# Kernel tuning notes

Measured on AMD Instinct MI355X. Metric: run time of the kernel, lower is better.

The kernel has to match this reference:

```python
import jax, jax.numpy as jnp
import numpy as np

D_MODEL = 768
N_HEADS = 12
HEAD = 64
B, T = 2, 2048


def setup_inputs() -> dict:
    key = jax.random.key(0)
    k1, k2, k3 = jax.random.split(key, 3)
    x = jax.random.normal(k1, (B, T, D_MODEL), dtype=jnp.float32)
    W1 = jax.random.normal(k2, (3 * D_MODEL, D_MODEL), dtype=jnp.float32) * (1.0 / np.sqrt(D_MODEL))
    b1 = jnp.zeros((3 * D_MODEL,), dtype=jnp.float32)
    W2 = jax.random.normal(k3, (D_MODEL, D_MODEL), dtype=jnp.float32) * (1.0 / np.sqrt(D_MODEL))
    b2 = jnp.zeros((D_MODEL,), dtype=jnp.float32)
    return {"x": x, "W1": W1, "b1": b1, "W2": W2, "b2": b2}


def reference(x, W1, b1, W2, b2):
    Bx, Tx, C = x.shape
    qkv = jnp.einsum('btc,fc->btf', x, W1) + b1            # (B,T,3C)
    q, k, v = jnp.split(qkv, 3, axis=-1)
    # (B,T,H,Dh) -> (B,H,T,Dh)
    q = q.reshape(Bx, Tx, N_HEADS, HEAD).transpose(0, 2, 1, 3)
    k = k.reshape(Bx, Tx, N_HEADS, HEAD).transpose(0, 2, 1, 3)
    v = v.reshape(Bx, Tx, N_HEADS, HEAD).transpose(0, 2, 1, 3)
    scale = 1.0 / np.sqrt(HEAD)
    scores = jnp.einsum('bhqd,bhkd->bhqk', q, k) * scale   # (B,H,T,T)
    causal = jnp.tril(jnp.ones((Tx, Tx), dtype=bool))
    scores = jnp.where(causal, scores, jnp.finfo(scores.dtype).min)
    attn = jax.nn.softmax(scores, axis=-1)
    o = jnp.einsum('bhqk,bhkd->bhqd', attn, v)             # (B,H,T,Dh)
    o = o.transpose(0, 2, 1, 3).reshape(Bx, Tx, C)
    return jnp.einsum('btc,fc->btf', o, W2) + b2
```

## Files before the change

### kernel.cpp

```cpp
#include <hip/hip_runtime.h>


typedef float f32x4 __attribute__((ext_vector_type(4)));
typedef __bf16 bf16x8 __attribute__((ext_vector_type(8)));

#define D_MODEL 768
#define F3 2304
#define NHEADS 12
#define HEAD 64
#define BB 2
#define TT 2048
#define MROWS (BB*TT)
#define KDIM 768
#define LOG2E 1.44269504f
#define NX (MROWS*D_MODEL)
#define NW1 (F3*KDIM)
#define NW2 (D_MODEL*KDIM)

__device__ __forceinline__ unsigned short f2bf(float f) {
    unsigned int u = __float_as_uint(f);
    u += 0x7fffu + ((u >> 16) & 1u);
    return (unsigned short)(u >> 16);
}
__device__ __forceinline__ unsigned int pack2bf(float a, float b) {
    unsigned int ua = __float_as_uint(a), ub = __float_as_uint(b);
    ua += 0x7fffu + ((ua >> 16) & 1u);
    ub += 0x7fffu + ((ub >> 16) & 1u);
    return (ua >> 16) | (ub & 0xffff0000u);
}

__device__ __forceinline__ void async_copy16(unsigned short* lds, const unsigned short* g) {
    __builtin_amdgcn_global_load_lds(
        (const __attribute__((address_space(1))) unsigned int*)(const void*)g,
        (__attribute__((address_space(3))) unsigned int*)(void*)lds,
        16, 0, 0);
}

__global__ void prep(const float* __restrict__ x, const float* __restrict__ W1,
                     const float* __restrict__ W2, unsigned short* __restrict__ xb,
                     unsigned short* __restrict__ w1b, unsigned short* __restrict__ w2b) {
    const int i4 = (blockIdx.x * blockDim.x + threadIdx.x) * 4;
    const float* src; unsigned short* dst; int off;
    if (i4 < NX)                { src = x;  dst = xb;  off = i4; }
    else if (i4 < NX + NW1)     { src = W1; dst = w1b; off = i4 - NX; }
    else if (i4 < NX + NW1 + NW2) { src = W2; dst = w2b; off = i4 - NX - NW1; }
    else return;
    float4 v = *(const float4*)(src + off);
    uint2 o;
    o.x = pack2bf(v.x, v.y);
    o.y = pack2bf(v.z, v.w);
    *(uint2*)(dst + off) = o;
}

template<int EPI>
__global__ __launch_bounds__(256, 4) void gemm_bt(
    const unsigned short* __restrict__ A, const unsigned short* __restrict__ Bw,
    const float* __restrict__ bias, int K,
    float* __restrict__ Cout,
    unsigned short* __restrict__ Qb, unsigned short* __restrict__ Kb,
    unsigned short* __restrict__ VT)
{
    __shared__ unsigned short As[128*64];
    __shared__ unsigned short Bs[128*64];
    const int tid  = threadIdx.x;
    const int wave = tid >> 6;
    const int lane = tid & 63;
    const int quad = lane >> 4;
    const int l16  = lane & 15;
    const int m0 = blockIdx.x * 128;
    const int n0 = blockIdx.y * 128;
    const int wm = (wave >> 1) * 64;
    const int wn = (wave & 1) * 64;

    f32x4 acc[4][4] = {};

    const unsigned short* Ablk = A + (size_t)m0 * K;
    const unsigned short* Bblk = Bw + (size_t)n0 * K;
    const int srow = (lane >> 3);
    const int scol = ((lane & 7) ^ srow) * 8;

    for (int k0 = 0; k0 < K; k0 += 64) {
        #pragma unroll
        for (int q2 = 0; q2 < 4; ++q2) {
            int t = wave * 4 + q2;
            int row = t * 8 + srow;
            async_copy16(As + t * 512, Ablk + (size_t)row * K + k0 + scol);
            async_copy16(Bs + t * 512, Bblk + (size_t)row * K + k0 + scol);
        }
        asm volatile("s_waitcnt vmcnt(0)" ::: "memory");
        __syncthreads();

        #pragma unroll
        for (int kc2 = 0; kc2 < 2; ++kc2) {
            const int pos = ((kc2*4 + quad) ^ (l16 & 7)) * 8;
            bf16x8 a[4], b[4];
            #pragma unroll
            for (int i = 0; i < 4; ++i)
                a[i] = *(const bf16x8*)(As + (wm + i*16 + l16)*64 + pos);
            #pragma unroll
            for (int j = 0; j < 4; ++j)
                b[j] = *(const bf16x8*)(Bs + (wn + j*16 + l16)*64 + pos);
            #pragma unroll
            for (int i = 0; i < 4; ++i)
                #pragma unroll
                for (int j = 0; j < 4; ++j)
                    acc[i][j] = __builtin_amdgcn_mfma_f32_16x16x32_bf16(a[i], b[j], acc[i][j], 0, 0, 0);
        }
        __syncthreads();
    }

    if (EPI == 1) {
        #pragma unroll
        for (int j = 0; j < 4; ++j) {
            const int n = n0 + wn + j*16 + l16;
            const float bv = bias[n];
            #pragma unroll
            for (int i = 0; i < 4; ++i)
                #pragma unroll
                for (int r = 0; r < 4; ++r) {
                    const int m = m0 + wm + i*16 + quad*4 + r;
                    Cout[(size_t)m * D_MODEL + n] = acc[i][j][r] + bv;
                }
        }
    } else {
        const int seg = blockIdx.y / 6;
        if (seg < 2) {
            #pragma unroll
            for (int j = 0; j < 4; ++j) {
                const int n = n0 + wn + j*16 + l16;
                const float bv = bias[n];
                const int f = n - seg * 768;
                const int h = f >> 6, d = f & 63;
                #pragma unroll
                for (int i = 0; i < 4; ++i)
                    #pragma unroll
                    for (int r = 0; r < 4; ++r) {
                        const int m = m0 + wm + i*16 + quad*4 + r;
                        const int b = m >> 11, t = m & 2047;
                        const size_t idx = (((size_t)(b*NHEADS + h)) * TT + t) * HEAD + d;
                        const float v = acc[i][j][r] + bv;
                        if (seg == 0) Qb[idx] = f2bf(v * (0.125f * LOG2E));
                        else          Kb[idx] = f2bf(v);
                    }
            }
        } else {
            #pragma unroll
            for (int j = 0; j < 4; ++j) {
                const int n = n0 + wn + j*16 + l16;
                const float bv = bias[n];
                const int f = n - 1536;
                const int h = f >> 6, d = f & 63;
                #pragma unroll
                for (int i = 0; i < 4; ++i) {
                    const int m = m0 + wm + i*16 + quad*4;
                    const int b = m >> 11, t = m & 2047;
                    uint2 pk;
                    pk.x = pack2bf(acc[i][j][0] + bv, acc[i][j][1] + bv);
                    pk.y = pack2bf(acc[i][j][2] + bv, acc[i][j][3] + bv);
                    *(uint2*)(VT + ((size_t)(b*NHEADS + h) * HEAD + d) * TT + t) = pk;
                }
            }
        }
    }
}

__global__ __launch_bounds__(256, 3) void attn(
    const unsigned short* __restrict__ Qb, const unsigned short* __restrict__ Kb,
    const unsigned short* __restrict__ VT, unsigned short* __restrict__ Ob)
{
    __shared__ unsigned short Ks[128*64];
    __shared__ unsigned short Vt[64*128];
    __shared__ unsigned short Ps[4][16*128];

    const int tid  = threadIdx.x;
    const int wave = tid >> 6;
    const int lane = tid & 63;
    const int quad = lane >> 4;
    const int l16  = lane & 15;
    const int qt = (blockIdx.x + blockIdx.y) & 15;
    const int bh = blockIdx.y;
    const size_t hbase = (size_t)bh * TT * HEAD;

    bf16x8 qreg[2][2];
    #pragma unroll
    for (int g = 0; g < 2; ++g) {
        const unsigned short* qp = Qb + hbase
            + (size_t)(qt*128 + g*64 + wave*16 + l16) * HEAD + quad*8;
        qreg[g][0] = *(const bf16x8*)(qp);
        qreg[g][1] = *(const bf16x8*)(qp + 32);
    }

    const int krow8 = tid >> 3;
    const int kchunk = ((tid & 7) ^ (krow8 & 7)) * 8;
    const int vrow16 = tid >> 4;
    const int vchunk = ((tid & 15) ^ (vrow16 & 7)) * 8;

    f32x4 oacc[2][4] = {};
    float lst[2] = {0.f, 0.f};
    const int nkt = qt + 1;

    for (int kt = 0; kt < nkt; ++kt) {
        __syncthreads();

        const unsigned short* ksrc = Kb + hbase + (size_t)kt * 128 * HEAD;
        #pragma unroll
        for (int i = 0; i < 4; ++i)
            async_copy16(Ks + i*2048 + tid*8,
                         ksrc + (size_t)(i*32 + krow8) * 64 + kchunk);
        const unsigned short* vsrc = VT + hbase + kt * 128;
        #pragma unroll
        for (int i = 0; i < 4; ++i)
            async_copy16(Vt + i*2048 + tid*8,
                         vsrc + (size_t)(i*16 + vrow16) * TT + vchunk);
        asm volatile("s_waitcnt vmcnt(0)" ::: "memory");
        __syncthreads();

        #pragma unroll
        for (int g = 0; g < 2; ++g) {
            f32x4 s[8] = {};
            #pragma unroll
            for (int kc2 = 0; kc2 < 2; ++kc2) {
                bf16x8 bq = qreg[g][kc2];
                const int pos = ((kc2*4 + quad) ^ (l16 & 7)) * 8;
                #pragma unroll
                for (int nt = 0; nt < 8; ++nt) {
                    bf16x8 ak = *(const bf16x8*)(Ks + (nt*16 + l16)*64 + pos);
                    s[nt] = __builtin_amdgcn_mfma_f32_16x16x32_bf16(ak, bq, s[nt], 0, 0, 0);
                }
            }

            if (kt == qt) {
                const int ql = g*64 + wave*16 + l16;
                #pragma unroll
                for (int nt = 0; nt < 8; ++nt)
                    #pragma unroll
                    for (int r = 0; r < 4; ++r)
                        if (nt*16 + quad*4 + r > ql) s[nt][r] = -1e30f;
            }

            float rsum = 0.f;
            uint2 pck[8];
            #pragma unroll
            for (int nt = 0; nt < 8; ++nt) {
                const float p0 = exp2f(s[nt][0]);
                const float p1 = exp2f(s[nt][1]);
                const float p2 = exp2f(s[nt][2]);
                const float p3 = exp2f(s[nt][3]);
                rsum += (p0 + p1) + (p2 + p3);
                pck[nt].x = (__float_as_uint(p0) >> 16) | (__float_as_uint(p1) & 0xffff0000u);
                pck[nt].y = (__float_as_uint(p2) >> 16) | (__float_as_uint(p3) & 0xffff0000u);
            }
            rsum += __shfl_xor(rsum, 16);
            rsum += __shfl_xor(rsum, 32);
            lst[g] += rsum;

            #pragma unroll
            for (int nt = 0; nt < 8; ++nt)
                *(uint2*)(&Ps[wave][l16*128
                    + ((nt*2 + (quad>>1)) ^ (l16 & 7))*8 + (quad&1)*4]) = pck[nt];

            #pragma unroll
            for (int kc = 0; kc < 4; ++kc) {
                const int pos = ((kc*4 + quad) ^ (l16 & 7)) * 8;
                bf16x8 ap = *(const bf16x8*)(&Ps[wave][l16*128 + pos]);
                #pragma unroll
                for (int dt = 0; dt < 4; ++dt) {
                    bf16x8 bv = *(const bf16x8*)(Vt + (dt*16 + l16)*128 + pos);
                    oacc[g][dt] = __builtin_amdgcn_mfma_f32_16x16x32_bf16(ap, bv, oacc[g][dt], 0, 0, 0);
                }
            }
        }
    }

    const int b = bh / NHEADS, h = bh % NHEADS;
    #pragma unroll
    for (int g = 0; g < 2; ++g) {
        const float linv = 1.0f / lst[g];
        float lr[4];
        #pragma unroll
        for (int r = 0; r < 4; ++r) lr[r] = __shfl(linv, quad*4 + r);
        #pragma unroll
        for (int r = 0; r < 4; ++r) {
            const int m = b * TT + qt*128 + g*64 + wave*16 + quad*4 + r;
            #pragma unroll
            for (int dt = 0; dt < 4; ++dt)
                Ob[(size_t)m * D_MODEL + h*HEAD + dt*16 + l16] = f2bf(oacc[g][dt][r] * lr[r]);
        }
    }
}

extern "C" void kernel_launch(void* const* d_in, const int* in_sizes, int n_in,
                              void* d_out, int out_size, void* d_ws, size_t ws_size,
                              hipStream_t stream) {
    const float* x  = (const float*)d_in[0];
    const float* W1 = (const float*)d_in[1];
    const float* b1 = (const float*)d_in[2];
    const float* W2 = (const float*)d_in[3];
    const float* b2 = (const float*)d_in[4];
    float* out = (float*)d_out;

    unsigned short* ws = (unsigned short*)d_ws;
    unsigned short* xb  = ws;
    unsigned short* w1b = xb  + (size_t)NX;
    unsigned short* w2b = w1b + (size_t)NW1;
    unsigned short* Qb  = w2b + (size_t)NW2;
    unsigned short* Kb  = Qb + (size_t)BB*NHEADS*TT*HEAD;
    unsigned short* VT  = Kb + (size_t)BB*NHEADS*TT*HEAD;
    unsigned short* Ob  = VT + (size_t)BB*NHEADS*TT*HEAD;

    prep<<<((NX + NW1 + NW2)/4 + 255)/256, 256, 0, stream>>>(x, W1, W2, xb, w1b, w2b);

    gemm_bt<0><<<dim3(MROWS/128, F3/128), 256, 0, stream>>>(
        xb, w1b, b1, KDIM, nullptr, Qb, Kb, VT);

    attn<<<dim3(TT/128, BB*NHEADS), 256, 0, stream>>>(Qb, Kb, VT, Ob);

    gemm_bt<1><<<dim3(MROWS/128, D_MODEL/128), 256, 0, stream>>>(
        Ob, w2b, b2, KDIM, out, nullptr, nullptr, nullptr);
}
```

Measured before the change: 177.9 us.

## Make attention waves independent, reading K/V directly from global memory

```diff
diff --git a/kernel.cpp b/kernel.cpp
--- a/kernel.cpp
+++ b/kernel.cpp
@@ -164,128 +164,103 @@
     }
 }
 
-__global__ __launch_bounds__(256, 3) void attn(
+__global__ __launch_bounds__(256, 4) void attn(
     const unsigned short* __restrict__ Qb, const unsigned short* __restrict__ Kb,
     const unsigned short* __restrict__ VT, unsigned short* __restrict__ Ob)
 {
-    __shared__ unsigned short Ks[128*64];
-    __shared__ unsigned short Vt[64*128];
-    __shared__ unsigned short Ps[4][16*128];
+    __shared__ unsigned short Ps[4][16*64];
 
     const int tid  = threadIdx.x;
     const int wave = tid >> 6;
     const int lane = tid & 63;
     const int quad = lane >> 4;
     const int l16  = lane & 15;
-    const int qt = (blockIdx.x + blockIdx.y) & 15;
     const int bh = blockIdx.y;
+    const int s  = wave*32 + ((blockIdx.x + blockIdx.y) & 31);
     const size_t hbase = (size_t)bh * TT * HEAD;
 
-    bf16x8 qreg[2][2];
+    unsigned short* ps = &Ps[wave][0];
+    const int psw = 2 * (l16 & 7);
+
+    bf16x8 q0, q1;
+    {
+        const unsigned short* qp = Qb + hbase + (size_t)(s*16 + l16) * HEAD + quad*8;
+        q0 = *(const bf16x8*)(qp);
+        q1 = *(const bf16x8*)(qp + 32);
+    }
+
+    f32x4 oacc[4] = {};
+    float lst = 0.f;
+    const int nkt = (s >> 2) + 1;
+
+    const unsigned short* kp0 = Kb + hbase + (size_t)l16 * HEAD + quad*8;
+    const unsigned short* vp0 = VT + hbase + (size_t)l16 * TT + quad*8;
+
+    for (int kt = 0; kt < nkt; ++kt) {
+        f32x4 sA[4] = {};
+        const unsigned short* kp = kp0 + (size_t)kt * 64 * HEAD;
+        #pragma unroll
+        for (int kc = 0; kc < 2; ++kc) {
+            const bf16x8 bq = kc ? q1 : q0;
+            #pragma unroll
+            for (int nt = 0; nt < 4; ++nt) {
+                bf16x8 ak = *(const bf16x8*)(kp + (size_t)nt*16*HEAD + kc*32);
+                sA[nt] = __builtin_amdgcn_mfma_f32_16x16x32_bf16(ak, bq, sA[nt], 0, 0, 0);
+            }
+        }
+
+        if (kt == nkt - 1) {
+            const int thr = s*16 + l16 - kt*64 - quad*4;
+            #pragma unroll
+            for (int nt = 0; nt < 4; ++nt)
+                #pragma unroll
+                for (int r = 0; r < 4; ++r)
+                    if (nt*16 + r > thr) sA[nt][r] = -1e30f;
+        }
+
+        float rsum = 0.f;
+        uint2 pck[4];
+        #pragma unroll
+        for (int nt = 0; nt < 4; ++nt) {
+            const float p0 = exp2f(sA[nt][0]);
+            const float p1 = exp2f(sA[nt][1]);
+            const float p2 = exp2f(sA[nt][2]);
+            const float p3 = exp2f(sA[nt][3]);
+            rsum += (p0 + p1) + (p2 + p3);
+            pck[nt].x = (__float_as_uint(p0) >> 16) | (__float_as_uint(p1) & 0xffff0000u);
+            pck[nt].y = (__float_as_uint(p2) >> 16) | (__float_as_uint(p3) & 0xffff0000u);
+        }
+        rsum += __shfl_xor(rsum, 16);
+        rsum += __shfl_xor(rsum, 32);
+        lst += rsum;
+
+        #pragma unroll
+        for (int nt = 0; nt < 4; ++nt)
+            *(uint2*)(ps + l16*64 + (((nt*4 + quad) ^ psw) * 4)) = pck[nt];
+
+        const unsigned short* vp = vp0 + kt*64;
+        #pragma unroll
+        for (int kc = 0; kc < 2; ++kc) {
+            bf16x8 ap = *(const bf16x8*)(ps + l16*64 + (((kc*8 + quad*2) ^ psw) * 4));
+            #pragma unroll
+            for (int dt = 0; dt < 4; ++dt) {
+                bf16x8 bv = *(const bf16x8*)(vp + (size_t)dt*16*TT + kc*32);
+                oacc[dt] = __builtin_amdgcn_mfma_f32_16x16x32_bf16(ap, bv, oacc[dt], 0, 0, 0);
+            }
+        }
+    }
+
+    const float linv = 1.0f / lst;
+    float lr[4];
     #pragma unroll
-    for (int g = 0; g < 2; ++g) {
-        const unsigned short* qp = Qb + hbase
-            + (size_t)(qt*128 + g*64 + wave*16 + l16) * HEAD + quad*8;
-        qreg[g][0] = *(const bf16x8*)(qp);
-        qreg[g][1] = *(const bf16x8*)(qp + 32);
-    }
-
-    const int krow8 = tid >> 3;
-    const int kchunk = ((tid & 7) ^ (krow8 & 7)) * 8;
-    const int vrow16 = tid >> 4;
-    const int vchunk = ((tid & 15) ^ (vrow16 & 7)) * 8;
-
-    f32x4 oacc[2][4] = {};
-    float lst[2] = {0.f, 0.f};
-    const int nkt = qt + 1;
-
-    for (int kt = 0; kt < nkt; ++kt) {
-        __syncthreads();
-
-        const unsigned short* ksrc = Kb + hbase + (size_t)kt * 128 * HEAD;
-        #pragma unroll
-        for (int i = 0; i < 4; ++i)
-            async_copy16(Ks + i*2048 + tid*8,
-                         ksrc + (size_t)(i*32 + krow8) * 64 + kchunk);
-        const unsigned short* vsrc = VT + hbase + kt * 128;
-        #pragma unroll
-        for (int i = 0; i < 4; ++i)
-            async_copy16(Vt + i*2048 + tid*8,
-                         vsrc + (size_t)(i*16 + vrow16) * TT + vchunk);
-        asm volatile("s_waitcnt vmcnt(0)" ::: "memory");
-        __syncthreads();
-
-        #pragma unroll
-        for (int g = 0; g < 2; ++g) {
-            f32x4 s[8] = {};
-            #pragma unroll
-            for (int kc2 = 0; kc2 < 2; ++kc2) {
-                bf16x8 bq = qreg[g][kc2];
-                const int pos = ((kc2*4 + quad) ^ (l16 & 7)) * 8;
-                #pragma unroll
-                for (int nt = 0; nt < 8; ++nt) {
-                    bf16x8 ak = *(const bf16x8*)(Ks + (nt*16 + l16)*64 + pos);
-                    s[nt] = __builtin_amdgcn_mfma_f32_16x16x32_bf16(ak, bq, s[nt], 0, 0, 0);
-                }
-            }
-
-            if (kt == qt) {
-                const int ql = g*64 + wave*16 + l16;
-                #pragma unroll
-                for (int nt = 0; nt < 8; ++nt)
-                    #pragma unroll
-                    for (int r = 0; r < 4; ++r)
-                        if (nt*16 + quad*4 + r > ql) s[nt][r] = -1e30f;
-            }
-
-            float rsum = 0.f;
-            uint2 pck[8];
-            #pragma unroll
-            for (int nt = 0; nt < 8; ++nt) {
-                const float p0 = exp2f(s[nt][0]);
-                const float p1 = exp2f(s[nt][1]);
-                const float p2 = exp2f(s[nt][2]);
-                const float p3 = exp2f(s[nt][3]);
-                rsum += (p0 + p1) + (p2 + p3);
-                pck[nt].x = (__float_as_uint(p0) >> 16) | (__float_as_uint(p1) & 0xffff0000u);
-                pck[nt].y = (__float_as_uint(p2) >> 16) | (__float_as_uint(p3) & 0xffff0000u);
-            }
-            rsum += __shfl_xor(rsum, 16);
-            rsum += __shfl_xor(rsum, 32);
-            lst[g] += rsum;
-
-            #pragma unroll
-            for (int nt = 0; nt < 8; ++nt)
-                *(uint2*)(&Ps[wave][l16*128
-                    + ((nt*2 + (quad>>1)) ^ (l16 & 7))*8 + (quad&1)*4]) = pck[nt];
-
-            #pragma unroll
-            for (int kc = 0; kc < 4; ++kc) {
-                const int pos = ((kc*4 + quad) ^ (l16 & 7)) * 8;
-                bf16x8 ap = *(const bf16x8*)(&Ps[wave][l16*128 + pos]);
-                #pragma unroll
-                for (int dt = 0; dt < 4; ++dt) {
-                    bf16x8 bv = *(const bf16x8*)(Vt + (dt*16 + l16)*128 + pos);
-                    oacc[g][dt] = __builtin_amdgcn_mfma_f32_16x16x32_bf16(ap, bv, oacc[g][dt], 0, 0, 0);
-                }
-            }
-        }
-    }
-
+    for (int r = 0; r < 4; ++r) lr[r] = __shfl(linv, quad*4 + r);
     const int b = bh / NHEADS, h = bh % NHEADS;
     #pragma unroll
-    for (int g = 0; g < 2; ++g) {
-        const float linv = 1.0f / lst[g];
-        float lr[4];
-        #pragma unroll
-        for (int r = 0; r < 4; ++r) lr[r] = __shfl(linv, quad*4 + r);
-        #pragma unroll
-        for (int r = 0; r < 4; ++r) {
-            const int m = b * TT + qt*128 + g*64 + wave*16 + quad*4 + r;
-            #pragma unroll
-            for (int dt = 0; dt < 4; ++dt)
-                Ob[(size_t)m * D_MODEL + h*HEAD + dt*16 + l16] = f2bf(oacc[g][dt][r] * lr[r]);
-        }
+    for (int r = 0; r < 4; ++r) {
+        const int m = b * TT + s*16 + quad*4 + r;
+        #pragma unroll
+        for (int dt = 0; dt < 4; ++dt)
+            Ob[(size_t)m * D_MODEL + h*HEAD + dt*16 + l16] = f2bf(oacc[dt][r] * lr[r]);
     }
 }
 
@@ -313,7 +288,7 @@
     gemm_bt<0><<<dim3(MROWS/128, F3/128), 256, 0, stream>>>(
         xb, w1b, b1, KDIM, nullptr, Qb, Kb, VT);
 
-    attn<<<dim3(TT/128, BB*NHEADS), 256, 0, stream>>>(Qb, Kb, VT, Ob);
+    attn<<<dim3(32, BB*NHEADS), 256, 0, stream>>>(Qb, Kb, VT, Ob);
 
     gemm_bt<1><<<dim3(MROWS/128, D_MODEL/128), 256, 0, stream>>>(
         Ob, w2b, b2, KDIM, out, nullptr, nullptr, nullptr);
```

New measurement: 211.9 us. 19.1% more time.

## Halve attention and output GEMM tile heights to raise block count

Applied to the files above, without the earlier changes.

```diff
diff --git a/kernel.cpp b/kernel.cpp
--- a/kernel.cpp
+++ b/kernel.cpp
@@ -52,11 +52,9 @@
     *(uint2*)(dst + off) = o;
 }
 
-template<int EPI>
-__global__ __launch_bounds__(256, 4) void gemm_bt(
+__global__ __launch_bounds__(256, 4) void gemm1(
     const unsigned short* __restrict__ A, const unsigned short* __restrict__ Bw,
     const float* __restrict__ bias, int K,
-    float* __restrict__ Cout,
     unsigned short* __restrict__ Qb, unsigned short* __restrict__ Kb,
     unsigned short* __restrict__ VT)
 {
@@ -109,62 +107,115 @@
         __syncthreads();
     }
 
-    if (EPI == 1) {
+    const int seg = blockIdx.y / 6;
+    if (seg < 2) {
         #pragma unroll
         for (int j = 0; j < 4; ++j) {
             const int n = n0 + wn + j*16 + l16;
             const float bv = bias[n];
+            const int f = n - seg * 768;
+            const int h = f >> 6, d = f & 63;
             #pragma unroll
             for (int i = 0; i < 4; ++i)
                 #pragma unroll
                 for (int r = 0; r < 4; ++r) {
                     const int m = m0 + wm + i*16 + quad*4 + r;
-                    Cout[(size_t)m * D_MODEL + n] = acc[i][j][r] + bv;
+                    const int b = m >> 11, t = m & 2047;
+                    const size_t idx = (((size_t)(b*NHEADS + h)) * TT + t) * HEAD + d;
+                    const float v = acc[i][j][r] + bv;
+                    if (seg == 0) Qb[idx] = f2bf(v * (0.125f * LOG2E));
+                    else          Kb[idx] = f2bf(v);
                 }
         }
     } else {
-        const int seg = blockIdx.y / 6;
-        if (seg < 2) {
-            #pragma unroll
-            for (int j = 0; j < 4; ++j) {
-                const int n = n0 + wn + j*16 + l16;
-                const float bv = bias[n];
-                const int f = n - seg * 768;
-                const int h = f >> 6, d = f & 63;
+        #pragma unroll
+        for (int j = 0; j < 4; ++j) {
+            const int n = n0 + wn + j*16 + l16;
+            const float bv = bias[n];
+            const int f = n - 1536;
+            const int h = f >> 6, d = f & 63;
+            #pragma unroll
+            for (int i = 0; i < 4; ++i) {
+                const int m = m0 + wm + i*16 + quad*4;
+                const int b = m >> 11, t = m & 2047;
+                uint2 pk;
+                pk.x = pack2bf(acc[i][j][0] + bv, acc[i][j][1] + bv);
+                pk.y = pack2bf(acc[i][j][2] + bv, acc[i][j][3] + bv);
+                *(uint2*)(VT + ((size_t)(b*NHEADS + h) * HEAD + d) * TT + t) = pk;
+            }
+        }
+    }
+}
+
+__global__ __launch_bounds__(256, 4) void gemm2(
+    const unsigned short* __restrict__ A, const unsigned short* __restrict__ Bw,
+    const float* __restrict__ bias, int K, float* __restrict__ Cout)
+{
+    __shared__ unsigned short As[64*64];
+    __shared__ unsigned short Bs[128*64];
+    const int tid  = threadIdx.x;
+    const int wave = tid >> 6;
+    const int lane = tid & 63;
+    const int quad = lane >> 4;
+    const int l16  = lane & 15;
+    const int m0 = blockIdx.x * 64;
+    const int n0 = blockIdx.y * 128;
+    const int wm = (wave >> 1) * 32;
+    const int wn = (wave & 1) * 64;
+
+    f32x4 acc[2][4] = {};
+
+    const unsigned short* Ablk = A + (size_t)m0 * K;
+    const unsigned short* Bblk = Bw + (size_t)n0 * K;
+    const int srow = tid >> 3;
+    const int scol = ((tid & 7) ^ (srow & 7)) * 8;
+
+    for (int k0 = 0; k0 < K; k0 += 64) {
+        #pragma unroll
+        for (int i = 0; i < 2; ++i)
+            async_copy16(As + i*2048 + tid*8,
+                         Ablk + (size_t)(i*32 + srow) * K + k0 + scol);
+        #pragma unroll
+        for (int i = 0; i < 4; ++i)
+            async_copy16(Bs + i*2048 + tid*8,
+                         Bblk + (size_t)(i*32 + srow) * K + k0 + scol);
+        asm volatile("s_waitcnt vmcnt(0)" ::: "memory");
+        __syncthreads();
+
+        #pragma unroll
+        for (int kc2 = 0; kc2 < 2; ++kc2) {
+            const int pos = ((kc2*4 + quad) ^ (l16 & 7)) * 8;
+            bf16x8 a[2], b[4];
+            #pragma unroll
+            for (int i = 0; i < 2; ++i)
+                a[i] = *(const bf16x8*)(As + (wm + i*16 + l16)*64 + pos);
+            #pragma unroll
+            for (int j = 0; j < 4; ++j)
+                b[j] = *(const bf16x8*)(Bs + (wn + j*16 + l16)*64 + pos);
+            #pragma unroll
+            for (int i = 0; i < 2; ++i)
                 #pragma unroll
-                for (int i = 0; i < 4; ++i)
-                    #pragma unroll
-                    for (int r = 0; r < 4; ++r) {
-                        const int m = m0 + wm + i*16 + quad*4 + r;
-                        const int b = m >> 11, t = m & 2047;
-                        const size_t idx = (((size_t)(b*NHEADS + h)) * TT + t) * HEAD + d;
-                        const float v = acc[i][j][r] + bv;
-                        if (seg == 0) Qb[idx] = f2bf(v * (0.125f * LOG2E));
-                        else          Kb[idx] = f2bf(v);
-                    }
+                for (int j = 0; j < 4; ++j)
+                    acc[i][j] = __builtin_amdgcn_mfma_f32_16x16x32_bf16(a[i], b[j], acc[i][j], 0, 0, 0);
+        }
+        __syncthreads();
+    }
+
+    #pragma unroll
+    for (int j = 0; j < 4; ++j) {
+        const int n = n0 + wn + j*16 + l16;
+        const float bv = bias[n];
+        #pragma unroll
+        for (int i = 0; i < 2; ++i)
+            #pragma unroll
+            for (int r = 0; r < 4; ++r) {
+                const int m = m0 + wm + i*16 + quad*4 + r;
+                Cout[(size_t)m * D_MODEL + n] = acc[i][j][r] + bv;
             }
-        } else {
-            #pragma unroll
-            for (int j = 0; j < 4; ++j) {
-                const int n = n0 + wn + j*16 + l16;
-                const float bv = bias[n];
-                const int f = n - 1536;
-                const int h = f >> 6, d = f & 63;
-                #pragma unroll
-                for (int i = 0; i < 4; ++i) {
-                    const int m = m0 + wm + i*16 + quad*4;
-                    const int b = m >> 11, t = m & 2047;
-                    uint2 pk;
-                    pk.x = pack2bf(acc[i][j][0] + bv, acc[i][j][1] + bv);
-                    pk.y = pack2bf(acc[i][j][2] + bv, acc[i][j][3] + bv);
-                    *(uint2*)(VT + ((size_t)(b*NHEADS + h) * HEAD + d) * TT + t) = pk;
-                }
-            }
-        }
-    }
-}
-
-__global__ __launch_bounds__(256, 3) void attn(
+    }
+}
+
+__global__ __launch_bounds__(256, 2) void attn(
     const unsigned short* __restrict__ Qb, const unsigned short* __restrict__ Kb,
     const unsigned short* __restrict__ VT, unsigned short* __restrict__ Ob)
 {
@@ -177,27 +228,26 @@
     const int lane = tid & 63;
     const int quad = lane >> 4;
     const int l16  = lane & 15;
-    const int qt = (blockIdx.x + blockIdx.y) & 15;
+    const int qt = (blockIdx.x + blockIdx.y) & 31;
     const int bh = blockIdx.y;
     const size_t hbase = (size_t)bh * TT * HEAD;
-
-    bf16x8 qreg[2][2];
-    #pragma unroll
-    for (int g = 0; g < 2; ++g) {
-        const unsigned short* qp = Qb + hbase
-            + (size_t)(qt*128 + g*64 + wave*16 + l16) * HEAD + quad*8;
-        qreg[g][0] = *(const bf16x8*)(qp);
-        qreg[g][1] = *(const bf16x8*)(qp + 32);
-    }
-
-    const int krow8 = tid >> 3;
-    const int kchunk = ((tid & 7) ^ (krow8 & 7)) * 8;
-    const int vrow16 = tid >> 4;
-    const int vchunk = ((tid & 15) ^ (vrow16 & 7)) * 8;
-
-    f32x4 oacc[2][4] = {};
-    float lst[2] = {0.f, 0.f};
-    const int nkt = qt + 1;
+    const int qg = qt*64 + wave*16 + l16;
+
+    bf16x8 qreg[2];
+    {
+        const unsigned short* qp = Qb + hbase + (size_t)qg * HEAD + quad*8;
+        qreg[0] = *(const bf16x8*)(qp);
+        qreg[1] = *(const bf16x8*)(qp + 32);
+    }
+
+    const int krow = tid >> 3;
+    const int kchunk = ((tid & 7) ^ (krow & 7)) * 8;
+    const int vrow = tid >> 4;
+    const int vchunk = ((tid & 15) ^ vrow) * 8;
+
+    f32x4 oacc[4] = {};
+    float lst = 0.f;
+    const int nkt = (qt >> 1) + 1;
 
     for (int kt = 0; kt < nkt; ++kt) {
         __syncthreads();
@@ -206,86 +256,78 @@
         #pragma unroll
         for (int i = 0; i < 4; ++i)
             async_copy16(Ks + i*2048 + tid*8,
-                         ksrc + (size_t)(i*32 + krow8) * 64 + kchunk);
-        const unsigned short* vsrc = VT + hbase + kt * 128;
+                         ksrc + (size_t)(i*32 + krow) * 64 + kchunk);
         #pragma unroll
         for (int i = 0; i < 4; ++i)
             async_copy16(Vt + i*2048 + tid*8,
-                         vsrc + (size_t)(i*16 + vrow16) * TT + vchunk);
+                         VT + hbase + (size_t)(i*16 + vrow) * TT + kt*128 + vchunk);
         asm volatile("s_waitcnt vmcnt(0)" ::: "memory");
         __syncthreads();
 
-        #pragma unroll
-        for (int g = 0; g < 2; ++g) {
-            f32x4 s[8] = {};
-            #pragma unroll
-            for (int kc2 = 0; kc2 < 2; ++kc2) {
-                bf16x8 bq = qreg[g][kc2];
-                const int pos = ((kc2*4 + quad) ^ (l16 & 7)) * 8;
+        f32x4 s[8] = {};
+        #pragma unroll
+        for (int kc2 = 0; kc2 < 2; ++kc2) {
+            bf16x8 bq = qreg[kc2];
+            const int pos = ((kc2*4 + quad) ^ (l16 & 7)) * 8;
+            #pragma unroll
+            for (int nt = 0; nt < 8; ++nt) {
+                bf16x8 ak = *(const bf16x8*)(Ks + (nt*16 + l16)*64 + pos);
+                s[nt] = __builtin_amdgcn_mfma_f32_16x16x32_bf16(ak, bq, s[nt], 0, 0, 0);
+            }
+        }
+
+        if (kt == nkt - 1) {
+            const int kq = kt*128 + quad*4;
+            #pragma unroll
+            for (int nt = 0; nt < 8; ++nt)
                 #pragma unroll
-                for (int nt = 0; nt < 8; ++nt) {
-                    bf16x8 ak = *(const bf16x8*)(Ks + (nt*16 + l16)*64 + pos);
-                    s[nt] = __builtin_amdgcn_mfma_f32_16x16x32_bf16(ak, bq, s[nt], 0, 0, 0);
-                }
+                for (int r = 0; r < 4; ++r)
+                    if (kq + nt*16 + r > qg) s[nt][r] = -1e30f;
+        }
+
+        float rsum = 0.f;
+        uint2 pck[8];
+        #pragma unroll
+        for (int nt = 0; nt < 8; ++nt) {
+            const float p0 = exp2f(s[nt][0]);
+            const float p1 = exp2f(s[nt][1]);
+            const float p2 = exp2f(s[nt][2]);
+            const float p3 = exp2f(s[nt][3]);
+            rsum += (p0 + p1) + (p2 + p3);
+            pck[nt].x = (__float_as_uint(p0) >> 16) | (__float_as_uint(p1) & 0xffff0000u);
+            pck[nt].y = (__float_as_uint(p2) >> 16) | (__float_as_uint(p3) & 0xffff0000u);
+        }
+        rsum += __shfl_xor(rsum, 16);
+        rsum += __shfl_xor(rsum, 32);
+        lst += rsum;
+
+        #pragma unroll
+        for (int nt = 0; nt < 8; ++nt)
+            *(uint2*)(&Ps[wave][l16*128 + ((nt*2 + (quad>>1)) ^ l16)*8 + (quad&1)*4]) = pck[nt];
+
+        #pragma unroll
+        for (int kc = 0; kc < 4; ++kc) {
+            bf16x8 ap = *(const bf16x8*)(&Ps[wave][l16*128 + ((kc*4 + quad) ^ l16)*8]);
+            const int vp = ((kc*4 + quad) ^ l16) * 8;
+            #pragma unroll
+            for (int dt = 0; dt < 4; ++dt) {
+                bf16x8 bv = *(const bf16x8*)(Vt + (dt*16 + l16)*128 + vp);
+                oacc[dt] = __builtin_amdgcn_mfma_f32_16x16x32_bf16(ap, bv, oacc[dt], 0, 0, 0);
             }
-
-            if (kt == qt) {
-                const int ql = g*64 + wave*16 + l16;
-                #pragma unroll
-                for (int nt = 0; nt < 8; ++nt)
-                    #pragma unroll
-                    for (int r = 0; r < 4; ++r)
-                        if (nt*16 + quad*4 + r > ql) s[nt][r] = -1e30f;
-            }
-
-            float rsum = 0.f;
-            uint2 pck[8];
-            #pragma unroll
-            for (int nt = 0; nt < 8; ++nt) {
-                const float p0 = exp2f(s[nt][0]);
-                const float p1 = exp2f(s[nt][1]);
-                const float p2 = exp2f(s[nt][2]);
-                const float p3 = exp2f(s[nt][3]);
-                rsum += (p0 + p1) + (p2 + p3);
-                pck[nt].x = (__float_as_uint(p0) >> 16) | (__float_as_uint(p1) & 0xffff0000u);
-                pck[nt].y = (__float_as_uint(p2) >> 16) | (__float_as_uint(p3) & 0xffff0000u);
-            }
-            rsum += __shfl_xor(rsum, 16);
-            rsum += __shfl_xor(rsum, 32);
-            lst[g] += rsum;
-
-            #pragma unroll
-            for (int nt = 0; nt < 8; ++nt)
-                *(uint2*)(&Ps[wave][l16*128
-                    + ((nt*2 + (quad>>1)) ^ (l16 & 7))*8 + (quad&1)*4]) = pck[nt];
-
-            #pragma unroll
-            for (int kc = 0; kc < 4; ++kc) {
-                const int pos = ((kc*4 + quad) ^ (l16 & 7)) * 8;
-                bf16x8 ap = *(const bf16x8*)(&Ps[wave][l16*128 + pos]);
-                #pragma unroll
-                for (int dt = 0; dt < 4; ++dt) {
-                    bf16x8 bv = *(const bf16x8*)(Vt + (dt*16 + l16)*128 + pos);
-                    oacc[g][dt] = __builtin_amdgcn_mfma_f32_16x16x32_bf16(ap, bv, oacc[g][dt], 0, 0, 0);
-                }
-            }
-        }
-    }
-
+        }
+    }
+
+    const float linv = 1.0f / lst;
+    float lr[4];
+    #pragma unroll
+    for (int r = 0; r < 4; ++r) lr[r] = __shfl(linv, quad*4 + r);
     const int b = bh / NHEADS, h = bh % NHEADS;
     #pragma unroll
-    for (int g = 0; g < 2; ++g) {
-        const float linv = 1.0f / lst[g];
-        float lr[4];
-        #pragma unroll
-        for (int r = 0; r < 4; ++r) lr[r] = __shfl(linv, quad*4 + r);
-        #pragma unroll
-        for (int r = 0; r < 4; ++r) {
-            const int m = b * TT + qt*128 + g*64 + wave*16 + quad*4 + r;
-            #pragma unroll
-            for (int dt = 0; dt < 4; ++dt)
-                Ob[(size_t)m * D_MODEL + h*HEAD + dt*16 + l16] = f2bf(oacc[g][dt][r] * lr[r]);
-        }
+    for (int r = 0; r < 4; ++r) {
+        const int m = b * TT + qt*64 + wave*16 + quad*4 + r;
+        #pragma unroll
+        for (int dt = 0; dt < 4; ++dt)
+            Ob[(size_t)m * D_MODEL + h*HEAD + dt*16 + l16] = f2bf(oacc[dt][r] * lr[r]);
     }
 }
 
@@ -310,11 +352,11 @@
 
     prep<<<((NX + NW1 + NW2)/4 + 255)/256, 256, 0, stream>>>(x, W1, W2, xb, w1b, w2b);
 
-    gemm_bt<0><<<dim3(MROWS/128, F3/128), 256, 0, stream>>>(
-        xb, w1b, b1, KDIM, nullptr, Qb, Kb, VT);
-
-    attn<<<dim3(TT/128, BB*NHEADS), 256, 0, stream>>>(Qb, Kb, VT, Ob);
-
-    gemm_bt<1><<<dim3(MROWS/128, D_MODEL/128), 256, 0, stream>>>(
-        Ob, w2b, b2, KDIM, out, nullptr, nullptr, nullptr);
-}
+    gemm1<<<dim3(MROWS/128, F3/128), 256, 0, stream>>>(
+        xb, w1b, b1, KDIM, Qb, Kb, VT);
+
+    attn<<<dim3(32, BB*NHEADS), 256, 0, stream>>>(Qb, Kb, VT, Ob);
+
+    gemm2<<<dim3(MROWS/64, D_MODEL/128), 256, 0, stream>>>(
+        Ob, w2b, b2, KDIM, out);
+}
```

Measured after the change: 152.8 us. 1.16x faster.
